# Kernel tuning notes

Hardware: AMD Instinct MI355X
Metric: run time of the kernel (lower is better)

The kernel has to match this reference:

```python
import jax, jax.numpy as jnp
import numpy as np

H, KB = 8, 8          # z_num grid (h, k)
OB, IB = 64, 64       # per-call weight block [OB, IB, K]
K, L = 9, 9           # kernel dims of exe_unet_weight and unet_1d_weights
ZD, PD, DH = 64, 16, 128  # z_dim, pde_inputs dim, hypernet hidden


def setup_inputs() -> dict:
    key = jax.random.key(0)
    k1, k2, k3, k4, k5 = jax.random.split(key, 5)
    # z params: torch.fmod(randn, 2) as in the original __init__
    z_all = jnp.fmod(jax.random.normal(k1, (H * KB, ZD), jnp.float32), 2.0)
    W1 = jax.random.normal(k2, (DH, ZD + PD), jnp.float32) * 0.1
    b1 = jnp.zeros((DH,), jnp.float32)
    W2 = jax.random.normal(k3, (OB * IB * K, DH), jnp.float32) * 0.02
    b2 = jnp.zeros((OB * IB * K,), jnp.float32)
    unet_1d_weights = jax.random.normal(k4, (H * OB, KB * IB, L), jnp.float32)
    pde_inputs = jax.random.normal(k5, (PD,), jnp.float32)
    return {"z_all": z_all, "W1": W1, "b1": b1, "W2": W2, "b2": b2,
            "unet_1d_weights": unet_1d_weights, "pde_inputs": pde_inputs}


def reference(z_all, W1, b1, W2, b2, unet_1d_weights, pde_inputs):
    # Batched hypernet: one GEMM over all h*k z vectors instead of h*k calls.
    x = jnp.concatenate([z_all, jnp.broadcast_to(pde_inputs, (H * KB, PD))], axis=1)  # [hk, ZD+PD]
    hid = jax.nn.relu(x @ W1.T + b1)                    # [hk, DH]
    w = (hid @ W2.T + b2).reshape(H, KB, OB, IB, K)      # per-cell blocks
    # cat(dim=1) within row, cat(dim=0) across rows -> [H*OB, KB*IB, K]
    exe_unet_weight = w.transpose(0, 2, 1, 3, 4).reshape(H * OB, KB * IB, K)
    # broadcast outer product over kernel dims
    w_2d = jnp.einsum('oik,oil->oikl', exe_unet_weight, unet_1d_weights)
    return w_2d
```

## Files before the change

kernel.cpp:

```cpp
#include <hip/hip_runtime.h>

#define ZD_ 64
#define PD_ 16
#define DH_ 128

__global__ void hid_kernel(const float* __restrict__ z_all,
                           const float* __restrict__ W1,
                           const float* __restrict__ b1,
                           const float* __restrict__ pde,
                           float* __restrict__ hidT) {
    int gid = blockIdx.x * 256 + threadIdx.x;
    int d = gid >> 6;
    int r = gid & 63;
    const float* w = W1 + d * (ZD_ + PD_);
    const float* z = z_all + r * ZD_;
    float acc = b1[d];
    #pragma unroll 8
    for (int c = 0; c < ZD_; ++c) acc += z[c] * w[c];
    #pragma unroll
    for (int c = 0; c < PD_; ++c) acc += pde[c] * w[ZD_ + c];
    hidT[d * 64 + r] = fmaxf(acc, 0.0f);
}

#define SMEM_FLOATS 18208

__global__ __launch_bounds__(256) void fused_kernel(
        const float* __restrict__ hidT,
        const float* __restrict__ W2,
        const float* __restrict__ b2,
        const float* __restrict__ unet,
        float* __restrict__ out) {
    __shared__ __align__(16) float smem[SMEM_FLOATS];
    float* s_w2 = smem;
    float* s_hT = smem + 9504;

    int tid = threadIdx.x;
    int b   = blockIdx.x;
    int ob  = b >> 3;
    int ibp = b & 7;
    int n0  = ob * 576 + ibp * 72;

    const float4* g4 = reinterpret_cast<const float4*>(W2 + (size_t)n0 * DH_);
    #pragma unroll
    for (int t = 0; t < 9; ++t) {
        int j   = t * 256 + tid;
        int row = j >> 5;
        int c4  = j & 31;
        *reinterpret_cast<float4*>(&s_w2[row * 132 + c4 * 4]) = g4[j];
    }
    const float4* h4g = reinterpret_cast<const float4*>(hidT);
    #pragma unroll
    for (int t = 0; t < 8; ++t) {
        int j  = t * 256 + tid;
        int d  = j >> 4;
        int r4 = j & 15;
        *reinterpret_cast<float4*>(&s_hT[d * 68 + r4 * 4]) = h4g[j];
    }

    int cg  = tid & 15;
    int ibl = (tid >> 4) & 7;
    int ks  = tid >> 7;

    float4 acc[9];
    if (ks == 0) {
        #pragma unroll
        for (int kk = 0; kk < 9; ++kk) {
            float bv = b2[n0 + ibl * 9 + kk];
            acc[kk] = make_float4(bv, bv, bv, bv);
        }
    } else {
        #pragma unroll
        for (int kk = 0; kk < 9; ++kk) acc[kk] = make_float4(0.f, 0.f, 0.f, 0.f);
    }
    __syncthreads();

    const float* wbase = s_w2 + ibl * 9 * 132 + ks * 64;
    const float* hbase = s_hT + (size_t)ks * 64 * 68 + 4 * cg;
    #pragma unroll 2
    for (int cc = 0; cc < 64; cc += 4) {
        float4 h0 = *reinterpret_cast<const float4*>(&hbase[(cc + 0) * 68]);
        float4 h1 = *reinterpret_cast<const float4*>(&hbase[(cc + 1) * 68]);
        float4 h2 = *reinterpret_cast<const float4*>(&hbase[(cc + 2) * 68]);
        float4 h3 = *reinterpret_cast<const float4*>(&hbase[(cc + 3) * 68]);
        #pragma unroll
        for (int kk = 0; kk < 9; ++kk) {
            float4 w = *reinterpret_cast<const float4*>(&wbase[kk * 132 + cc]);
            acc[kk].x += h0.x * w.x + h1.x * w.y + h2.x * w.z + h3.x * w.w;
            acc[kk].y += h0.y * w.x + h1.y * w.y + h2.y * w.z + h3.y * w.w;
            acc[kk].z += h0.z * w.x + h1.z * w.y + h2.z * w.z + h3.z * w.w;
            acc[kk].w += h0.w * w.x + h1.w * w.y + h2.w * w.z + h3.w * w.w;
        }
    }
    __syncthreads();

    float* s_exe = smem;
    float* s_red = smem + 4672;
    float* s_un  = smem + 9504;

    if (ks == 1) {
        int slot = tid & 127;
        #pragma unroll
        for (int kk = 0; kk < 9; ++kk) {
            s_red[slot * 37 + 0 * 9 + kk] = acc[kk].x;
            s_red[slot * 37 + 1 * 9 + kk] = acc[kk].y;
            s_red[slot * 37 + 2 * 9 + kk] = acc[kk].z;
            s_red[slot * 37 + 3 * 9 + kk] = acc[kk].w;
        }
    }
    for (int j = tid; j < 1152; j += 256) {
        int cell = j / 18;
        int q    = j - cell * 18;
        int hh = cell >> 3, kb = cell & 7;
        size_t gb = ((size_t)((hh * 64 + ob) * 512 + kb * 64 + ibp * 8)) * 9;
        *reinterpret_cast<float4*>(&s_un[cell * 72 + q * 4]) =
            *reinterpret_cast<const float4*>(unet + gb + q * 4);
    }
    __syncthreads();

    if (ks == 0) {
        #pragma unroll
        for (int kk = 0; kk < 9; ++kk) {
            int col = ibl * 9 + kk;
            s_exe[(4 * cg + 0) * 73 + col] = acc[kk].x + s_red[tid * 37 + 0 * 9 + kk];
            s_exe[(4 * cg + 1) * 73 + col] = acc[kk].y + s_red[tid * 37 + 1 * 9 + kk];
            s_exe[(4 * cg + 2) * 73 + col] = acc[kk].z + s_red[tid * 37 + 2 * 9 + kk];
            s_exe[(4 * cg + 3) * 73 + col] = acc[kk].w + s_red[tid * 37 + 3 * 9 + kk];
        }
    }
    __syncthreads();

    for (int idx = tid; idx < 10368; idx += 256) {
        int cell = idx / 162;
        int q    = idx - cell * 162;
        float4 v;
        float* vp = &v.x;
        #pragma unroll
        for (int j2 = 0; j2 < 4; ++j2) {
            int e    = q * 4 + j2;
            int ibl2 = e / 81;
            int rem  = e - ibl2 * 81;
            int k    = rem / 9;
            int l    = rem - k * 9;
            vp[j2] = s_exe[cell * 73 + ibl2 * 9 + k]
                   * s_un [cell * 72 + ibl2 * 9 + l];
        }
        int hh = cell >> 3, kb = cell & 7;
        size_t gb = ((size_t)((hh * 64 + ob) * 512 + kb * 64 + ibp * 8)) * 81;
        reinterpret_cast<float4*>(out + gb)[q] = v;
    }
}

extern "C" void kernel_launch(void* const* d_in, const int* in_sizes, int n_in,
                              void* d_out, int out_size, void* d_ws, size_t ws_size,
                              hipStream_t stream) {
    const float* z_all = (const float*)d_in[0];
    const float* W1    = (const float*)d_in[1];
    const float* b1    = (const float*)d_in[2];
    const float* W2    = (const float*)d_in[3];
    const float* b2    = (const float*)d_in[4];
    const float* unet  = (const float*)d_in[5];
    const float* pde   = (const float*)d_in[6];
    float* out = (float*)d_out;

    float* hidT = (float*)d_ws;

    hid_kernel<<<32, 256, 0, stream>>>(z_all, W1, b1, pde, hidT);
    fused_kernel<<<512, 256, 0, stream>>>(hidT, W2, b2, unet, out);
}
```

Measured before the change: 138.2 us.

## Halve per-block work to launch twice as many blocks with smaller smem

Result: slower. 148.8 us (+7.7%).

```diff
diff --git a/kernel.cpp b/kernel.cpp
--- a/kernel.cpp
+++ b/kernel.cpp
@@ -22,7 +22,7 @@
     hidT[d * 64 + r] = fmaxf(acc, 0.0f);
 }
 
-#define SMEM_FLOATS 18208
+#define SMEM_FLOATS 13456
 
 __global__ __launch_bounds__(256) void fused_kernel(
         const float* __restrict__ hidT,
@@ -32,21 +32,23 @@
         float* __restrict__ out) {
     __shared__ __align__(16) float smem[SMEM_FLOATS];
     float* s_w2 = smem;
-    float* s_hT = smem + 9504;
+    float* s_hT = smem + 4752;
 
     int tid = threadIdx.x;
     int b   = blockIdx.x;
-    int ob  = b >> 3;
-    int ibp = b & 7;
-    int n0  = ob * 576 + ibp * 72;
+    int ob  = b >> 4;
+    int ibp = b & 15;
+    int n0  = ob * 576 + ibp * 36;
 
     const float4* g4 = reinterpret_cast<const float4*>(W2 + (size_t)n0 * DH_);
     #pragma unroll
-    for (int t = 0; t < 9; ++t) {
-        int j   = t * 256 + tid;
-        int row = j >> 5;
-        int c4  = j & 31;
-        *reinterpret_cast<float4*>(&s_w2[row * 132 + c4 * 4]) = g4[j];
+    for (int t = 0; t < 5; ++t) {
+        int j = t * 256 + tid;
+        if (j < 1152) {
+            int row = j >> 5;
+            int c4  = j & 31;
+            *reinterpret_cast<float4*>(&s_w2[row * 132 + c4 * 4]) = g4[j];
+        }
     }
     const float4* h4g = reinterpret_cast<const float4*>(hidT);
     #pragma unroll
@@ -57,62 +59,58 @@
         *reinterpret_cast<float4*>(&s_hT[d * 68 + r4 * 4]) = h4g[j];
     }
 
-    int cg  = tid & 15;
-    int ibl = (tid >> 4) & 7;
+    int cp  = tid & 31;
+    int ibl = (tid >> 5) & 3;
     int ks  = tid >> 7;
 
-    float4 acc[9];
+    float2 acc[9];
     if (ks == 0) {
         #pragma unroll
         for (int kk = 0; kk < 9; ++kk) {
             float bv = b2[n0 + ibl * 9 + kk];
-            acc[kk] = make_float4(bv, bv, bv, bv);
+            acc[kk] = make_float2(bv, bv);
         }
     } else {
         #pragma unroll
-        for (int kk = 0; kk < 9; ++kk) acc[kk] = make_float4(0.f, 0.f, 0.f, 0.f);
+        for (int kk = 0; kk < 9; ++kk) acc[kk] = make_float2(0.f, 0.f);
     }
     __syncthreads();
 
     const float* wbase = s_w2 + ibl * 9 * 132 + ks * 64;
-    const float* hbase = s_hT + (size_t)ks * 64 * 68 + 4 * cg;
-    #pragma unroll 2
+    const float* hbase = s_hT + ks * 64 * 68 + 2 * cp;
+    #pragma unroll 4
     for (int cc = 0; cc < 64; cc += 4) {
-        float4 h0 = *reinterpret_cast<const float4*>(&hbase[(cc + 0) * 68]);
-        float4 h1 = *reinterpret_cast<const float4*>(&hbase[(cc + 1) * 68]);
-        float4 h2 = *reinterpret_cast<const float4*>(&hbase[(cc + 2) * 68]);
-        float4 h3 = *reinterpret_cast<const float4*>(&hbase[(cc + 3) * 68]);
+        float2 h0 = *reinterpret_cast<const float2*>(&hbase[(cc + 0) * 68]);
+        float2 h1 = *reinterpret_cast<const float2*>(&hbase[(cc + 1) * 68]);
+        float2 h2 = *reinterpret_cast<const float2*>(&hbase[(cc + 2) * 68]);
+        float2 h3 = *reinterpret_cast<const float2*>(&hbase[(cc + 3) * 68]);
         #pragma unroll
         for (int kk = 0; kk < 9; ++kk) {
             float4 w = *reinterpret_cast<const float4*>(&wbase[kk * 132 + cc]);
             acc[kk].x += h0.x * w.x + h1.x * w.y + h2.x * w.z + h3.x * w.w;
             acc[kk].y += h0.y * w.x + h1.y * w.y + h2.y * w.z + h3.y * w.w;
-            acc[kk].z += h0.z * w.x + h1.z * w.y + h2.z * w.z + h3.z * w.w;
-            acc[kk].w += h0.w * w.x + h1.w * w.y + h2.w * w.z + h3.w * w.w;
         }
     }
     __syncthreads();
 
     float* s_exe = smem;
-    float* s_red = smem + 4672;
-    float* s_un  = smem + 9504;
+    float* s_red = smem + 2368;
+    float* s_un  = smem + 4816;
 
     if (ks == 1) {
         int slot = tid & 127;
         #pragma unroll
         for (int kk = 0; kk < 9; ++kk) {
-            s_red[slot * 37 + 0 * 9 + kk] = acc[kk].x;
-            s_red[slot * 37 + 1 * 9 + kk] = acc[kk].y;
-            s_red[slot * 37 + 2 * 9 + kk] = acc[kk].z;
-            s_red[slot * 37 + 3 * 9 + kk] = acc[kk].w;
+            s_red[slot * 19 + kk]     = acc[kk].x;
+            s_red[slot * 19 + 9 + kk] = acc[kk].y;
         }
     }
-    for (int j = tid; j < 1152; j += 256) {
-        int cell = j / 18;
-        int q    = j - cell * 18;
+    for (int j = tid; j < 576; j += 256) {
+        int cell = j / 9;
+        int q    = j - cell * 9;
         int hh = cell >> 3, kb = cell & 7;
-        size_t gb = ((size_t)((hh * 64 + ob) * 512 + kb * 64 + ibp * 8)) * 9;
-        *reinterpret_cast<float4*>(&s_un[cell * 72 + q * 4]) =
+        size_t gb = ((size_t)((hh * 64 + ob) * 512 + kb * 64 + ibp * 4)) * 9;
+        *reinterpret_cast<float4*>(&s_un[cell * 36 + q * 4]) =
             *reinterpret_cast<const float4*>(unet + gb + q * 4);
     }
     __syncthreads();
@@ -121,17 +119,15 @@
         #pragma unroll
         for (int kk = 0; kk < 9; ++kk) {
             int col = ibl * 9 + kk;
-            s_exe[(4 * cg + 0) * 73 + col] = acc[kk].x + s_red[tid * 37 + 0 * 9 + kk];
-            s_exe[(4 * cg + 1) * 73 + col] = acc[kk].y + s_red[tid * 37 + 1 * 9 + kk];
-            s_exe[(4 * cg + 2) * 73 + col] = acc[kk].z + s_red[tid * 37 + 2 * 9 + kk];
-            s_exe[(4 * cg + 3) * 73 + col] = acc[kk].w + s_red[tid * 37 + 3 * 9 + kk];
+            s_exe[(2 * cp + 0) * 37 + col] = acc[kk].x + s_red[tid * 19 + kk];
+            s_exe[(2 * cp + 1) * 37 + col] = acc[kk].y + s_red[tid * 19 + 9 + kk];
         }
     }
     __syncthreads();
 
-    for (int idx = tid; idx < 10368; idx += 256) {
-        int cell = idx / 162;
-        int q    = idx - cell * 162;
+    for (int idx = tid; idx < 5184; idx += 256) {
+        int cell = idx / 81;
+        int q    = idx - cell * 81;
         float4 v;
         float* vp = &v.x;
         #pragma unroll
@@ -141,11 +137,11 @@
             int rem  = e - ibl2 * 81;
             int k    = rem / 9;
             int l    = rem - k * 9;
-            vp[j2] = s_exe[cell * 73 + ibl2 * 9 + k]
-                   * s_un [cell * 72 + ibl2 * 9 + l];
+            vp[j2] = s_exe[cell * 37 + ibl2 * 9 + k]
+                   * s_un [cell * 36 + ibl2 * 9 + l];
         }
         int hh = cell >> 3, kb = cell & 7;
-        size_t gb = ((size_t)((hh * 64 + ob) * 512 + kb * 64 + ibp * 8)) * 81;
+        size_t gb = ((size_t)((hh * 64 + ob) * 512 + kb * 64 + ibp * 4)) * 81;
         reinterpret_cast<float4*>(out + gb)[q] = v;
     }
 }
@@ -165,5 +161,5 @@
     float* hidT = (float*)d_ws;
 
     hid_kernel<<<32, 256, 0, stream>>>(z_all, W1, b1, pde, hidT);
-    fused_kernel<<<512, 256, 0, stream>>>(hidT, W2, b2, unet, out);
+    fused_kernel<<<1024, 256, 0, stream>>>(hidT, W2, b2, unet, out);
 }
```
